# Kernel optimization log

Measured on AMD Instinct MI355X. Metric: run time of the kernel, lower is better.

The kernel has to match this reference:

```python
import jax, jax.numpy as jnp
import numpy as np

BETA = 0.95      # leak
THRESH = 1.0     # snntorch Leaky default threshold
ALPHA = 2.0      # ATan surrogate alpha (atan_with_alpha)
T = 100          # SPIKE_STEPS
D_IN = 65536     # input_dims
HID = 256        # fc1 hidden (hardcoded)
N_OUT = 20       # n_actions(2) * NUM_NEURONS_PER_ACTION(10)


def spike_fn(x):
    # forward of snntorch surrogate.ATan: Heaviside
    return (x > 0.0).astype(x.dtype)


def lif_step(mem, cur):
    # snntorch Leaky, reset_mechanism='subtract':
    # reset computed from previous membrane (detached), then decay+integrate, then fire
    reset = jax.lax.stop_gradient((mem > THRESH).astype(mem.dtype))
    mem_new = BETA * mem + cur - reset * THRESH
    spk = spike_fn(mem_new - THRESH)
    return spk, mem_new


def _run_net(x, W1, b1, W2, b2):
    # x: [T, D_IN]. Precompute all layer-1 currents as one big GEMM, then scan the recurrence.
    cur1_all = x @ W1.T + b1  # [T, HID]

    def step(carry, cur1):
        mem1, mem2 = carry
        spk1, mem1 = lif_step(mem1, cur1)
        cur2 = spk1 @ W2.T + b2  # [n_out]
        spk2, mem2 = lif_step(mem2, cur2)
        return (mem1, mem2), spk2

    init = (jnp.zeros((W1.shape[0],), x.dtype), jnp.zeros((W2.shape[0],), x.dtype))
    (_, mem2_final), spk2_hist = jax.lax.scan(step, init, cur1_all)
    return spk2_hist, mem2_final  # [T, n_out], [n_out]


def setup_inputs() -> dict:
    key = jax.random.key(0)
    ks = jax.random.split(key, 5)
    s = 0.01
    return {
        "poisson_spikes": jax.random.uniform(ks[0], (T, 1, D_IN), dtype=jnp.float32),
        "aW1": jax.random.normal(ks[1], (HID, D_IN), dtype=jnp.float32) * s,
        "ab1": jnp.zeros((HID,), jnp.float32),
        "aW2": jax.random.normal(ks[2], (N_OUT, HID), dtype=jnp.float32) * s,
        "ab2": jnp.zeros((N_OUT,), jnp.float32),
        "cW1": jax.random.normal(ks[3], (HID, D_IN), dtype=jnp.float32) * s,
        "cb1": jnp.zeros((HID,), jnp.float32),
        "cW2": jax.random.normal(ks[4], (1, HID), dtype=jnp.float32) * s,
        "cb2": jnp.zeros((1,), jnp.float32),
    }


def reference(poisson_spikes, aW1, ab1, aW2, ab2, cW1, cb1, cW2, cb2):
    x = poisson_spikes[:, 0, :]  # effective batch of 1 -> [T, D_IN]
    actor_spk_hist, _ = _run_net(x, aW1, ab1, aW2, ab2)        # [T, 20]
    _, critic_mem = _run_net(x, cW1, cb1, cW2, cb2)            # [1]
    spk_sum = actor_spk_hist.sum(axis=0)                       # [20] (sum over timesteps)
    action_vals = jnp.stack([spk_sum[:10].sum(), spk_sum[10:].sum()])
    policy = jax.nn.softmax(action_vals)                       # [2]
    return policy, critic_mem
```

## Files before the change

kernel.cpp:

```cpp
#include <hip/hip_runtime.h>
#include <hip/hip_bf16.h>

#define T_STEPS 100
#define D_IN    65536
#define HID     256
#define HTOT    512
#define BETA    0.95f
#define THRESH  1.0f
#define CHUNK   256
#define ROWS    128

typedef __bf16 bf16x8 __attribute__((ext_vector_type(8)));
typedef float  f32x16 __attribute__((ext_vector_type(16)));

__global__ __launch_bounds__(1024, 4) void k_gemm1(
    const float* __restrict__ x,
    const float* __restrict__ aW1,
    const float* __restrict__ cW1,
    float* __restrict__ P,
    int Kc)
{
    const int half = blockIdx.x;
    const int s    = blockIdx.y;
    const int tid  = threadIdx.x;
    const int lane = tid & 63;
    const int l31  = lane & 31;
    const int wv   = tid >> 6;
    const int wt   = (wv & 1) * 64;
    const int hq   = (wv >> 1) * 32;

    __shared__ __bf16 Ah[ROWS][CHUNK];
    __shared__ __bf16 Am[ROWS][CHUNK];

    const float* Wsrc = half ? cW1 : aW1;
    const float* w0 = Wsrc + (size_t)(hq + l31) * D_IN + (lane >> 5) * 8;

    const int sr = tid >> 3;
    const float* xrow = x + (size_t)sr * D_IN + (tid & 7) * 8;
    const bool xok = (sr < T_STEPS);

    f32x16 acc0, acc1;
#pragma unroll
    for (int i = 0; i < 16; i++) { acc0[i] = 0.f; acc1[i] = 0.f; }

    const int k0      = s * Kc;
    const int nchunks = Kc / CHUNK;

    for (int c = 0; c < nchunks; c++) {
        const int kb = k0 + c * CHUNK;
        if (c) __syncthreads();
#pragma unroll
        for (int j = 0; j < 4; j++) {
            float4 v0 = make_float4(0.f, 0.f, 0.f, 0.f), v1 = v0;
            if (xok) {
                v0 = *(const float4*)(xrow + kb + j * 64);
                v1 = *(const float4*)(xrow + kb + j * 64 + 4);
            }
            float f[8] = {v0.x, v0.y, v0.z, v0.w, v1.x, v1.y, v1.z, v1.w};
            bf16x8 hi, mi;
#pragma unroll
            for (int e = 0; e < 8; e++) {
                __bf16 h = (__bf16)f[e];
                hi[e] = h; mi[e] = (__bf16)(f[e] - (float)h);
            }
            const int slot = (tid & 7) + j * 8;
            const int pe   = ((slot ^ (sr & 7)) << 3);
            *(bf16x8*)&Ah[sr][pe] = hi;
            *(bf16x8*)&Am[sr][pe] = mi;
        }
        __syncthreads();

        float4 bd0[3], bd1[3];
#define LOADB(i, sn) do {                                                     \
    const float* p_ = w0 + kb + (sn) * 16;                                    \
    bd0[i] = *(const float4*)p_;                                              \
    bd1[i] = *(const float4*)(p_ + 4);                                        \
} while (0)
        LOADB(0, 0);
        LOADB(1, 1);
#pragma unroll
        for (int s16 = 0; s16 < 16; s16++) {
            if (s16 + 2 < 16) LOADB((s16 + 2) % 3, s16 + 2);
            const int bi = s16 % 3;
            float f0_[8] = {bd0[bi].x, bd0[bi].y, bd0[bi].z, bd0[bi].w,
                            bd1[bi].x, bd1[bi].y, bd1[bi].z, bd1[bi].w};
            bf16x8 bh, bm;
#pragma unroll
            for (int e = 0; e < 8; e++) {
                __bf16 h = (__bf16)f0_[e];
                bh[e] = h; bm[e] = (__bf16)(f0_[e] - (float)h);
            }
            const int slot = s16 * 2 + (lane >> 5);
            const int r0 = wt + l31, r1 = r0 + 32;
            const int pe0 = ((slot ^ (r0 & 7)) << 3);
            const int pe1 = ((slot ^ (r1 & 7)) << 3);
            bf16x8 a0h = *(const bf16x8*)&Ah[r0][pe0];
            bf16x8 a0m = *(const bf16x8*)&Am[r0][pe0];
            bf16x8 a1h = *(const bf16x8*)&Ah[r1][pe1];
            bf16x8 a1m = *(const bf16x8*)&Am[r1][pe1];
            acc0 = __builtin_amdgcn_mfma_f32_32x32x16_bf16(a0m, bh, acc0, 0, 0, 0);
            acc0 = __builtin_amdgcn_mfma_f32_32x32x16_bf16(a0h, bm, acc0, 0, 0, 0);
            acc0 = __builtin_amdgcn_mfma_f32_32x32x16_bf16(a0h, bh, acc0, 0, 0, 0);
            acc1 = __builtin_amdgcn_mfma_f32_32x32x16_bf16(a1m, bh, acc1, 0, 0, 0);
            acc1 = __builtin_amdgcn_mfma_f32_32x32x16_bf16(a1h, bm, acc1, 0, 0, 0);
            acc1 = __builtin_amdgcn_mfma_f32_32x32x16_bf16(a1h, bh, acc1, 0, 0, 0);
        }
#undef LOADB
    }

    const int rbase = 4 * (lane >> 5);
    const int hcol  = half * 256 + hq + l31;
    float* Pb = P + (size_t)s * T_STEPS * HTOT;
#pragma unroll
    for (int reg = 0; reg < 16; reg++) {
        const int row = (reg & 3) + rbase + 8 * (reg >> 2);
        const int t0  = wt + row;
        const int t1  = wt + 32 + row;
        if (t0 < T_STEPS) Pb[(size_t)t0 * HTOT + hcol] = acc0[reg];
        if (t1 < T_STEPS) Pb[(size_t)t1 * HTOT + hcol] = acc1[reg];
    }
}

__global__ __launch_bounds__(256) void k_reduce(
    const float* __restrict__ P,
    const float* __restrict__ ab1, const float* __restrict__ cb1,
    float* __restrict__ cur1, int NS)
{
    int g4 = blockIdx.x * 256 + threadIdx.x;
    int g  = g4 * 4;
    int h0 = g & (HTOT - 1);
    float4 sum;
    sum.x = (h0 + 0 < HID) ? ab1[h0 + 0] : cb1[h0 + 0 - HID];
    sum.y = (h0 + 1 < HID) ? ab1[h0 + 1] : cb1[h0 + 1 - HID];
    sum.z = (h0 + 2 < HID) ? ab1[h0 + 2] : cb1[h0 + 2 - HID];
    sum.w = (h0 + 3 < HID) ? ab1[h0 + 3] : cb1[h0 + 3 - HID];
    for (int ss = 0; ss < NS; ss++) {
        float4 v = *(const float4*)(P + (size_t)ss * T_STEPS * HTOT + g);
        sum.x += v.x; sum.y += v.y; sum.z += v.z; sum.w += v.w;
    }
    *(float4*)(cur1 + g) = sum;
}

__global__ __launch_bounds__(64) void k_lif1(
    const float* __restrict__ cur1,
    unsigned long long* __restrict__ bitsws,
    float* __restrict__ wsa)
{
    const int b    = blockIdx.x;
    const int lane = threadIdx.x;
    const int n    = b * 64 + lane;

    float mem = 0.f;
    for (int tb = 0; tb < T_STEPS; tb += 10) {
        float c[10];
#pragma unroll
        for (int i = 0; i < 10; i++) c[i] = cur1[(size_t)(tb + i) * HTOT + n];
#pragma unroll
        for (int i = 0; i < 10; i++) {
            float reset = (mem > THRESH) ? THRESH : 0.f;
            mem = BETA * mem + c[i] - reset;
            unsigned long long m = __ballot(mem > THRESH);
            if (lane == 0) bitsws[(size_t)(tb + i) * 8 + b] = m;
        }
    }
    if (b == 0 && lane == 0) { wsa[0] = 0.f; wsa[1] = 0.f; }
}

__global__ __launch_bounds__(128) void k_gemm2(
    const unsigned long long* __restrict__ bitsws,
    const float* __restrict__ aW2, const float* __restrict__ ab2,
    const float* __restrict__ cW2, const float* __restrict__ cb2,
    float* __restrict__ wsa, float* __restrict__ out)
{
    const int j   = blockIdx.x;
    const int tid = threadIdx.x;

    __shared__ float W[256];
    __shared__ float c2[T_STEPS];

    const float* Wsrc = (j < 20) ? (aW2 + j * 256) : cW2;
    for (int i = tid; i < 256; i += 128) W[i] = Wsrc[i];
    const float bias  = (j < 20) ? ab2[j] : cb2[0];
    const int   wbase = (j < 20) ? 0 : 4;
    __syncthreads();

    const int t = tid;
    if (t < T_STEPS) {
        unsigned long long m0 = bitsws[(size_t)t * 8 + wbase + 0];
        unsigned long long m1 = bitsws[(size_t)t * 8 + wbase + 1];
        unsigned long long m2 = bitsws[(size_t)t * 8 + wbase + 2];
        unsigned long long m3 = bitsws[(size_t)t * 8 + wbase + 3];
        float acc = bias;
#pragma unroll
        for (int bitp = 0; bitp < 64; bitp++) {
            acc += ((m0 >> bitp) & 1ULL) ? W[bitp]       : 0.f;
            acc += ((m1 >> bitp) & 1ULL) ? W[64 + bitp]  : 0.f;
            acc += ((m2 >> bitp) & 1ULL) ? W[128 + bitp] : 0.f;
            acc += ((m3 >> bitp) & 1ULL) ? W[192 + bitp] : 0.f;
        }
        c2[t] = acc;
    }
    __syncthreads();

    if (tid == 0) {
        float mem = 0.f, spk = 0.f;
        for (int tt = 0; tt < T_STEPS; tt++) {
            float reset = (mem > THRESH) ? THRESH : 0.f;
            mem = BETA * mem + c2[tt] - reset;
            spk += (mem > THRESH) ? 1.f : 0.f;
        }
        if (j < 10)       atomicAdd(&wsa[0], spk);
        else if (j < 20)  atomicAdd(&wsa[1], spk);
        else              out[2] = mem;
    }
}

__global__ __launch_bounds__(64) void k_final(
    const float* __restrict__ wsa, float* __restrict__ out)
{
    if (threadIdx.x == 0) {
        float a0 = wsa[0], a1 = wsa[1];
        float mx = fmaxf(a0, a1);
        float e0 = expf(a0 - mx), e1 = expf(a1 - mx);
        float inv = 1.f / (e0 + e1);
        out[0] = e0 * inv;
        out[1] = e1 * inv;
    }
}

extern "C" void kernel_launch(void* const* d_in, const int* in_sizes, int n_in,
                              void* d_out, int out_size, void* d_ws, size_t ws_size,
                              hipStream_t stream) {
    const float* x   = (const float*)d_in[0];
    const float* aW1 = (const float*)d_in[1];
    const float* ab1 = (const float*)d_in[2];
    const float* aW2 = (const float*)d_in[3];
    const float* ab2 = (const float*)d_in[4];
    const float* cW1 = (const float*)d_in[5];
    const float* cb1 = (const float*)d_in[6];
    const float* cW2 = (const float*)d_in[7];
    const float* cb2 = (const float*)d_in[8];
    float* out = (float*)d_out;

    int NS = 128;
    while (NS > 8 &&
           ((size_t)(NS + 1) * T_STEPS * HTOT) * sizeof(float) + 8192 > ws_size)
        NS >>= 1;
    int Kc = D_IN / NS;

    float* P    = (float*)d_ws;
    float* cur1 = P + (size_t)NS * T_STEPS * HTOT;
    unsigned long long* bitsws =
        (unsigned long long*)(cur1 + T_STEPS * HTOT);
    float* wsa  = (float*)(bitsws + T_STEPS * 8);

    k_gemm1 <<<dim3(2, NS), 1024, 0, stream>>>(x, aW1, cW1, P, Kc);
    k_reduce<<<(T_STEPS * HTOT / 4) / 256, 256, 0, stream>>>(P, ab1, cb1, cur1, NS);
    k_lif1  <<<8, 64, 0, stream>>>(cur1, bitsws, wsa);
    k_gemm2 <<<21, 128, 0, stream>>>(bitsws, aW2, ab2, cW2, cb2, wsa, out);
    k_final <<<1, 64, 0, stream>>>(wsa, out);
}
```

Baseline: 99.07 us.

## Stream W1 tiles into LDS with async global_load_lds double buffering

Rewrites the layer-1 GEMM kernel so W1 is staged into a double-buffered shared-memory tile using direct global-to-LDS loads, overlapping the next tile's fetch with MFMA compute on the current one. Blocks shrink to 512 threads covering 128 hidden units each, giving four column tiles per K-split instead of two, and the K chunk drops to 64. This targets global-load latency on the dominant 2x65536x256 weight stream. In exchange, x is now loaded and split into bf16 hi/lo twice as often per block, and there are more barriers per chunk.

```diff
diff --git a/kernel.cpp b/kernel.cpp
--- a/kernel.cpp
+++ b/kernel.cpp
@@ -7,20 +7,26 @@
 #define HTOT    512
 #define BETA    0.95f
 #define THRESH  1.0f
-#define CHUNK   256
+#define CHUNK   64
 #define ROWS    128
 
 typedef __bf16 bf16x8 __attribute__((ext_vector_type(8)));
 typedef float  f32x16 __attribute__((ext_vector_type(16)));
 
-__global__ __launch_bounds__(1024, 4) void k_gemm1(
+__device__ __forceinline__ void gload_lds16(const float* g, void* l) {
+    __builtin_amdgcn_global_load_lds(
+        (const __attribute__((address_space(1))) void*)g,
+        (__attribute__((address_space(3))) void*)l, 16, 0, 0);
+}
+
+__global__ __launch_bounds__(512, 4) void k_gemm1(
     const float* __restrict__ x,
     const float* __restrict__ aW1,
     const float* __restrict__ cW1,
     float* __restrict__ P,
     int Kc)
 {
-    const int half = blockIdx.x;
+    const int ht   = blockIdx.x;
     const int s    = blockIdx.y;
     const int tid  = threadIdx.x;
     const int lane = tid & 63;
@@ -31,85 +37,114 @@
 
     __shared__ __bf16 Ah[ROWS][CHUNK];
     __shared__ __bf16 Am[ROWS][CHUNK];
-
-    const float* Wsrc = half ? cW1 : aW1;
-    const float* w0 = Wsrc + (size_t)(hq + l31) * D_IN + (lane >> 5) * 8;
-
-    const int sr = tid >> 3;
-    const float* xrow = x + (size_t)sr * D_IN + (tid & 7) * 8;
+    __shared__ float  Wf[2][128][32];
+
+    const float* Wbase = (ht < 2) ? (aW1 + (size_t)ht * 128 * D_IN)
+                                  : (cW1 + (size_t)(ht - 2) * 128 * D_IN);
+
+    const int gi0   = wv * 64 + lane;
+    const int wrow0 = gi0 >> 3,          wg0 = gi0 & 7;
+    const int wrow1 = (gi0 + 512) >> 3,  wg1 = (gi0 + 512) & 7;
+    const float* wsrc0 = Wbase + (size_t)wrow0 * D_IN + ((wg0 ^ (wrow0 & 7)) * 4);
+    const float* wsrc1 = Wbase + (size_t)wrow1 * D_IN + ((wg1 ^ (wrow1 & 7)) * 4);
+    char* WfB = (char*)&Wf[0][0][0];
+
+#define WSTAGE(buf, kflt) do {                                                \
+    gload_lds16(wsrc0 + (kflt), WfB + (buf) * 16384 + gi0 * 16);              \
+    gload_lds16(wsrc1 + (kflt), WfB + (buf) * 16384 + 8192 + gi0 * 16);       \
+} while (0)
+
+    const int sr = tid >> 2;
+    const int gq = tid & 3;
+    const float* xrow = x + (size_t)sr * D_IN + gq * 16;
     const bool xok = (sr < T_STEPS);
 
+#define XSTAGE(kflt) do {                                                     \
+    _Pragma("unroll")                                                         \
+    for (int j = 0; j < 2; j++) {                                             \
+        float4 v0 = make_float4(0.f, 0.f, 0.f, 0.f), v1 = v0;                 \
+        if (xok) {                                                            \
+            v0 = *(const float4*)(xrow + (kflt) + j * 8);                     \
+            v1 = *(const float4*)(xrow + (kflt) + j * 8 + 4);                 \
+        }                                                                     \
+        float f[8] = {v0.x, v0.y, v0.z, v0.w, v1.x, v1.y, v1.z, v1.w};        \
+        bf16x8 hi, mi;                                                        \
+        _Pragma("unroll")                                                     \
+        for (int e = 0; e < 8; e++) {                                         \
+            __bf16 h = (__bf16)f[e];                                          \
+            hi[e] = h; mi[e] = (__bf16)(f[e] - (float)h);                     \
+        }                                                                     \
+        const int slot = gq * 2 + j;                                          \
+        const int pe   = ((slot ^ (sr & 7)) << 3);                            \
+        *(bf16x8*)&Ah[sr][pe] = hi;                                           \
+        *(bf16x8*)&Am[sr][pe] = mi;                                           \
+    }                                                                         \
+} while (0)
+
     f32x16 acc0, acc1;
 #pragma unroll
     for (int i = 0; i < 16; i++) { acc0[i] = 0.f; acc1[i] = 0.f; }
+
+#define COMPUTE(buf, bk) do {                                                 \
+    _Pragma("unroll")                                                         \
+    for (int s16 = 0; s16 < 2; s16++) {                                       \
+        const int hr = hq + l31;                                              \
+        const int gb = s16 * 4 + (lane >> 5) * 2;                             \
+        const int g0 = (gb ^ (hr & 7));                                       \
+        const int g1 = ((gb + 1) ^ (hr & 7));                                 \
+        float4 wa = *(const float4*)&Wf[buf][hr][g0 * 4];                     \
+        float4 wb = *(const float4*)&Wf[buf][hr][g1 * 4];                     \
+        float fb[8] = {wa.x, wa.y, wa.z, wa.w, wb.x, wb.y, wb.z, wb.w};       \
+        bf16x8 bh, bm;                                                        \
+        _Pragma("unroll")                                                     \
+        for (int e = 0; e < 8; e++) {                                         \
+            __bf16 h = (__bf16)fb[e];                                         \
+            bh[e] = h; bm[e] = (__bf16)(fb[e] - (float)h);                    \
+        }                                                                     \
+        const int slot = (bk) * 4 + s16 * 2 + (lane >> 5);                    \
+        const int r0 = wt + l31, r1 = r0 + 32;                                \
+        const int pe0 = ((slot ^ (r0 & 7)) << 3);                             \
+        const int pe1 = ((slot ^ (r1 & 7)) << 3);                             \
+        bf16x8 a0h = *(const bf16x8*)&Ah[r0][pe0];                            \
+        bf16x8 a0m = *(const bf16x8*)&Am[r0][pe0];                            \
+        bf16x8 a1h = *(const bf16x8*)&Ah[r1][pe1];                            \
+        bf16x8 a1m = *(const bf16x8*)&Am[r1][pe1];                            \
+        acc0 = __builtin_amdgcn_mfma_f32_32x32x16_bf16(a0m, bh, acc0, 0,0,0); \
+        acc0 = __builtin_amdgcn_mfma_f32_32x32x16_bf16(a0h, bm, acc0, 0,0,0); \
+        acc0 = __builtin_amdgcn_mfma_f32_32x32x16_bf16(a0h, bh, acc0, 0,0,0); \
+        acc1 = __builtin_amdgcn_mfma_f32_32x32x16_bf16(a1m, bh, acc1, 0,0,0); \
+        acc1 = __builtin_amdgcn_mfma_f32_32x32x16_bf16(a1h, bm, acc1, 0,0,0); \
+        acc1 = __builtin_amdgcn_mfma_f32_32x32x16_bf16(a1h, bh, acc1, 0,0,0); \
+    }                                                                         \
+} while (0)
 
     const int k0      = s * Kc;
     const int nchunks = Kc / CHUNK;
 
+    WSTAGE(0, k0);
     for (int c = 0; c < nchunks; c++) {
-        const int kb = k0 + c * CHUNK;
-        if (c) __syncthreads();
-#pragma unroll
-        for (int j = 0; j < 4; j++) {
-            float4 v0 = make_float4(0.f, 0.f, 0.f, 0.f), v1 = v0;
-            if (xok) {
-                v0 = *(const float4*)(xrow + kb + j * 64);
-                v1 = *(const float4*)(xrow + kb + j * 64 + 4);
-            }
-            float f[8] = {v0.x, v0.y, v0.z, v0.w, v1.x, v1.y, v1.z, v1.w};
-            bf16x8 hi, mi;
-#pragma unroll
-            for (int e = 0; e < 8; e++) {
-                __bf16 h = (__bf16)f[e];
-                hi[e] = h; mi[e] = (__bf16)(f[e] - (float)h);
-            }
-            const int slot = (tid & 7) + j * 8;
-            const int pe   = ((slot ^ (sr & 7)) << 3);
-            *(bf16x8*)&Ah[sr][pe] = hi;
-            *(bf16x8*)&Am[sr][pe] = mi;
-        }
-        __syncthreads();
-
-        float4 bd0[3], bd1[3];
-#define LOADB(i, sn) do {                                                     \
-    const float* p_ = w0 + kb + (sn) * 16;                                    \
-    bd0[i] = *(const float4*)p_;                                              \
-    bd1[i] = *(const float4*)(p_ + 4);                                        \
-} while (0)
-        LOADB(0, 0);
-        LOADB(1, 1);
-#pragma unroll
-        for (int s16 = 0; s16 < 16; s16++) {
-            if (s16 + 2 < 16) LOADB((s16 + 2) % 3, s16 + 2);
-            const int bi = s16 % 3;
-            float f0_[8] = {bd0[bi].x, bd0[bi].y, bd0[bi].z, bd0[bi].w,
-                            bd1[bi].x, bd1[bi].y, bd1[bi].z, bd1[bi].w};
-            bf16x8 bh, bm;
-#pragma unroll
-            for (int e = 0; e < 8; e++) {
-                __bf16 h = (__bf16)f0_[e];
-                bh[e] = h; bm[e] = (__bf16)(f0_[e] - (float)h);
-            }
-            const int slot = s16 * 2 + (lane >> 5);
-            const int r0 = wt + l31, r1 = r0 + 32;
-            const int pe0 = ((slot ^ (r0 & 7)) << 3);
-            const int pe1 = ((slot ^ (r1 & 7)) << 3);
-            bf16x8 a0h = *(const bf16x8*)&Ah[r0][pe0];
-            bf16x8 a0m = *(const bf16x8*)&Am[r0][pe0];
-            bf16x8 a1h = *(const bf16x8*)&Ah[r1][pe1];
-            bf16x8 a1m = *(const bf16x8*)&Am[r1][pe1];
-            acc0 = __builtin_amdgcn_mfma_f32_32x32x16_bf16(a0m, bh, acc0, 0, 0, 0);
-            acc0 = __builtin_amdgcn_mfma_f32_32x32x16_bf16(a0h, bm, acc0, 0, 0, 0);
-            acc0 = __builtin_amdgcn_mfma_f32_32x32x16_bf16(a0h, bh, acc0, 0, 0, 0);
-            acc1 = __builtin_amdgcn_mfma_f32_32x32x16_bf16(a1m, bh, acc1, 0, 0, 0);
-            acc1 = __builtin_amdgcn_mfma_f32_32x32x16_bf16(a1h, bm, acc1, 0, 0, 0);
-            acc1 = __builtin_amdgcn_mfma_f32_32x32x16_bf16(a1h, bh, acc1, 0, 0, 0);
-        }
-#undef LOADB
-    }
+        const int kc = k0 + c * CHUNK;
+        asm volatile("s_waitcnt vmcnt(0)" ::: "memory");
+        __builtin_amdgcn_s_barrier();
+        __builtin_amdgcn_sched_barrier(0);
+        XSTAGE(kc);
+        asm volatile("s_waitcnt lgkmcnt(0)" ::: "memory");
+        __builtin_amdgcn_s_barrier();
+        __builtin_amdgcn_sched_barrier(0);
+        WSTAGE(1, kc + 32);
+        COMPUTE(0, 0);
+        asm volatile("s_waitcnt vmcnt(0)" ::: "memory");
+        __builtin_amdgcn_s_barrier();
+        __builtin_amdgcn_sched_barrier(0);
+        if (c + 1 < nchunks) WSTAGE(0, kc + CHUNK);
+        COMPUTE(1, 1);
+    }
+#undef WSTAGE
+#undef XSTAGE
+#undef COMPUTE
 
     const int rbase = 4 * (lane >> 5);
-    const int hcol  = half * 256 + hq + l31;
+    const int hcol  = ht * 128 + hq + l31;
     float* Pb = P + (size_t)s * T_STEPS * HTOT;
 #pragma unroll
     for (int reg = 0; reg < 16; reg++) {
@@ -254,7 +289,7 @@
         (unsigned long long*)(cur1 + T_STEPS * HTOT);
     float* wsa  = (float*)(bitsws + T_STEPS * 8);
 
-    k_gemm1 <<<dim3(2, NS), 1024, 0, stream>>>(x, aW1, cW1, P, Kc);
+    k_gemm1 <<<dim3(4, NS), 512, 0, stream>>>(x, aW1, cW1, P, Kc);
     k_reduce<<<(T_STEPS * HTOT / 4) / 256, 256, 0, stream>>>(P, ab1, cb1, cur1, NS);
     k_lif1  <<<8, 64, 0, stream>>>(cur1, bitsws, wsa);
     k_gemm2 <<<21, 128, 0, stream>>>(bitsws, aW2, ab2, cW2, cb2, wsa, out);
```

New measurement: 97.17 us. Within noise of the previous version (-1.9%).
